# Kernel tuning notes

Measured on AMD Instinct MI355X. Metric: run time of the kernel, lower is better.

The kernel has to match this reference:

```python
import jax, jax.numpy as jnp
import numpy as np

EMBED = 8      # embed_dim == n_qubits == d_k (forced by reshapes in the source)
FFN = 2048
LN_EPS = 1e-5


def _layernorm(x, g, b):
    mu = jnp.mean(x, axis=-1, keepdims=True)
    var = jnp.mean(jnp.square(x - mu), axis=-1, keepdims=True)
    return (x - mu) * jax.lax.rsqrt(var + LN_EPS) * g + b


def _quantum_measure(theta):
    # RX(theta_i) on each wire of |0..0>, CNOT ladder 0->1->...->n-1,
    # then <Z_i>. Closed form: <Z_i> = prod_{j<=i} cos(theta_j).
    return jnp.cumprod(jnp.cos(theta), axis=-1)


def setup_inputs() -> dict:
    key = jax.random.key(0)
    ks = jax.random.split(key, 8)
    B, S = 32, 4096
    s_e = 1.0 / np.sqrt(EMBED)
    s_f = 1.0 / np.sqrt(FFN)
    return {
        "x": jax.random.normal(ks[0], (B, S, EMBED), jnp.float32),
        "Wq": jax.random.uniform(ks[1], (EMBED, EMBED), jnp.float32, -s_e, s_e),
        "Wo": jax.random.uniform(ks[2], (EMBED, EMBED), jnp.float32, -s_e, s_e),
        "W1": jax.random.uniform(ks[3], (FFN, EMBED), jnp.float32, -s_e, s_e),
        "b1": jax.random.uniform(ks[4], (FFN,), jnp.float32, -s_e, s_e),
        "W2": jax.random.uniform(ks[5], (EMBED, FFN), jnp.float32, -s_f, s_f),
        "b2": jax.random.uniform(ks[6], (EMBED,), jnp.float32, -s_f, s_f),
        "g1": jnp.ones((EMBED,), jnp.float32),
        "beta1": jnp.zeros((EMBED,), jnp.float32),
        "g2": jnp.ones((EMBED,), jnp.float32),
        "beta2": jnp.zeros((EMBED,), jnp.float32),
    }


def reference(x, Wq, Wo, W1, b1, W2, b2, g1, beta1, g2, beta2):
    # Quantum multi-head attention (num_heads=1, d_k=n_wires=8).
    # Note: k_proj / v_proj outputs are unused in the original forward.
    q = jnp.einsum("bse,fe->bsf", x, Wq)          # (B,S,E)
    attn = jnp.einsum("bse,fe->bsf", _quantum_measure(q), Wo)
    h = _layernorm(x + attn, g1, beta1)           # dropout is identity (eval)
    # Quantum feed-forward: measure -> linear1 -> relu -> linear2
    m = _quantum_measure(h)                       # (B,S,E)
    hid = jax.nn.relu(jnp.einsum("bse,fe->bsf", m, W1) + b1)  # (B,S,FFN)
    ffn = jnp.einsum("bsf,ef->bse", hid, W2) + b2
    return _layernorm(h + ffn, g2, beta2)
```

## Files before the change

### kernel.cpp

```cpp
#include <hip/hip_runtime.h>
#include <hip/hip_bf16.h>

#define FFN 2048
#define LN_EPS 1e-5f

typedef __attribute__((ext_vector_type(8))) short bf16x8;
typedef __attribute__((ext_vector_type(4))) float f32x4;

union FragU { bf16x8 v; unsigned u[4]; uint4 q; };

static __device__ __forceinline__ unsigned cvtpk(float lo, float hi) {
    unsigned r;
    asm("v_cvt_pk_bf16_f32 %0, %1, %2" : "=v"(r) : "v"(lo), "v"(hi));
    return r;
}

static __device__ __forceinline__ unsigned pkrelu(unsigned a, unsigned z) {
    unsigned r;
    asm("v_pk_max_f16 %0, %1, %2" : "=v"(r) : "v"(a), "v"(z));
    return r;
}

static __device__ __forceinline__ ushort to_bf16(float f) {
    unsigned u = __float_as_uint(f);
    u += 0x7fffu + ((u >> 16) & 1u);
    return (ushort)(u >> 16);
}

__global__ __launch_bounds__(256) void tbq_prep(
    const float* __restrict__ W1, const float* __restrict__ b1,
    const float* __restrict__ W2, uint4* __restrict__ ws)
{
    const int idx = blockIdx.x * 256 + threadIdx.x;
    ushort v[8] = {0,0,0,0,0,0,0,0};
    if (idx < 8192) {
        const int lane = idx & 63, s = (idx >> 6) & 1, cc = idx >> 7;
        const int c = lane & 15, g = lane >> 4;
        const int f = cc * 32 + s * 16 + c;
        if (g == 0) {
            #pragma unroll
            for (int j = 0; j < 8; ++j) v[j] = to_bf16(W1[f * 8 + j]);
        } else if (g == 1) {
            v[0] = to_bf16(b1[f]);
        }
    } else {
        const int i2 = idx - 8192;
        const int lane = i2 & 63, cc = i2 >> 6;
        const int c = lane & 15, g = lane >> 4;
        if (c < 8) {
            #pragma unroll
            for (int j = 0; j < 8; ++j) {
                const int fl = 4 * g + (j & 3) + 16 * (j >> 2);
                v[j] = to_bf16(W2[c * FFN + cc * 32 + fl]);
            }
        }
    }
    union { ushort s[8]; uint4 q; } pk;
    #pragma unroll
    for (int j = 0; j < 8; ++j) pk.s[j] = v[j];
    ws[idx] = pk.q;
}

__global__ __launch_bounds__(256) void tbq_mfma(
    const float* __restrict__ x,
    const float* __restrict__ Wq,
    const float* __restrict__ Wo,
    const float* __restrict__ b2,
    const float* __restrict__ g1,
    const float* __restrict__ beta1,
    const float* __restrict__ g2,
    const float* __restrict__ beta2,
    const uint4* __restrict__ ws,
    float* __restrict__ out)
{
    __shared__ __align__(16) uint4 mS[64];
    __shared__ __align__(16) float part[4][64][8];

    const int tid  = threadIdx.x;
    const int lane = tid & 63;
    const int wv   = tid >> 6;
    const int c    = lane & 15;
    const int g    = lane >> 4;
    const int t    = blockIdx.x * 64 + lane;

    const uint4* fw1 = ws + lane;
    const uint4* fw2 = ws + 8192 + lane;
    const int cc0 = wv * 16;

    FragU F0[2], F1[2], A2[2];
    F0[0].q = fw1[cc0 * 128];
    F1[0].q = fw1[cc0 * 128 + 64];
    A2[0].q = fw2[cc0 * 64];

    float h[8];
    if (wv == 0) {
        const float4* xr = (const float4*)(x + (size_t)t * 8);
        float4 xa = xr[0], xb = xr[1];
        float xv[8] = {xa.x, xa.y, xa.z, xa.w, xb.x, xb.y, xb.z, xb.w};

        float qm[8];
        {
            float cp = 1.0f;
            #pragma unroll
            for (int f = 0; f < 8; ++f) {
                float acc = 0.0f;
                #pragma unroll
                for (int e = 0; e < 8; ++e) acc += xv[e] * Wq[f * 8 + e];
                cp *= __cosf(acc);
                qm[f] = cp;
            }
        }
        float mu = 0.0f;
        #pragma unroll
        for (int f = 0; f < 8; ++f) {
            float acc = 0.0f;
            #pragma unroll
            for (int e = 0; e < 8; ++e) acc += qm[e] * Wo[f * 8 + e];
            h[f] = xv[f] + acc;
            mu += h[f];
        }
        mu *= 0.125f;
        float var = 0.0f;
        #pragma unroll
        for (int i = 0; i < 8; ++i) { float d = h[i] - mu; var += d * d; }
        var *= 0.125f;
        float rs = rsqrtf(var + LN_EPS);
        #pragma unroll
        for (int i = 0; i < 8; ++i) h[i] = (h[i] - mu) * rs * g1[i] + beta1[i];

        float m[8];
        {
            float cp = 1.0f;
            #pragma unroll
            for (int i = 0; i < 8; ++i) { cp *= __cosf(h[i]); m[i] = cp; }
        }
        uint4 mq;
        mq.x = cvtpk(m[0], m[1]); mq.y = cvtpk(m[2], m[3]);
        mq.z = cvtpk(m[4], m[5]); mq.w = cvtpk(m[6], m[7]);
        mS[lane] = mq;
    }
    __syncthreads();

    FragU B1[4];
    #pragma unroll
    for (int T = 0; T < 4; ++T) {
        uint4 mr = mS[T * 16 + c];
        B1[T].u[0] = (g == 0) ? mr.x : ((g == 1) ? 0x00003F80u : 0u);
        B1[T].u[1] = (g == 0) ? mr.y : 0u;
        B1[T].u[2] = (g == 0) ? mr.z : 0u;
        B1[T].u[3] = (g == 0) ? mr.w : 0u;
    }

    f32x4 acc[4] = {{0,0,0,0},{0,0,0,0},{0,0,0,0},{0,0,0,0}};
    const unsigned zz = 0u;

    #pragma unroll
    for (int i = 0; i < 16; ++i) {
        const int cur = i & 1, nxt = cur ^ 1;
        if (i < 15) {
            F0[nxt].q = fw1[(cc0 + i + 1) * 128];
            F1[nxt].q = fw1[(cc0 + i + 1) * 128 + 64];
            A2[nxt].q = fw2[(cc0 + i + 1) * 64];
        }
        #pragma unroll
        for (int T = 0; T < 4; ++T) {
            f32x4 z = {0, 0, 0, 0};
            f32x4 c0 = __builtin_amdgcn_mfma_f32_16x16x32_bf16(F0[cur].v, B1[T].v, z, 0, 0, 0);
            f32x4 c1 = __builtin_amdgcn_mfma_f32_16x16x32_bf16(F1[cur].v, B1[T].v, z, 0, 0, 0);
            FragU B2;
            B2.u[0] = pkrelu(cvtpk(c0[0], c0[1]), zz);
            B2.u[1] = pkrelu(cvtpk(c0[2], c0[3]), zz);
            B2.u[2] = pkrelu(cvtpk(c1[0], c1[1]), zz);
            B2.u[3] = pkrelu(cvtpk(c1[2], c1[3]), zz);
            acc[T] = __builtin_amdgcn_mfma_f32_16x16x32_bf16(A2[cur].v, B2.v, acc[T], 0, 0, 0);
        }
    }

    if (g < 2) {
        #pragma unroll
        for (int T = 0; T < 4; ++T) {
            *(f32x4*)&part[wv][T * 16 + c][4 * g] = acc[T];
        }
    }
    __syncthreads();

    if (wv == 0) {
        float ffnv[8];
        #pragma unroll
        for (int e = 0; e < 8; ++e)
            ffnv[e] = part[0][lane][e] + part[1][lane][e]
                    + part[2][lane][e] + part[3][lane][e];

        float o[8];
        float mu2 = 0.0f;
        #pragma unroll
        for (int i = 0; i < 8; ++i) { o[i] = h[i] + ffnv[i] + b2[i]; mu2 += o[i]; }
        mu2 *= 0.125f;
        float v2 = 0.0f;
        #pragma unroll
        for (int i = 0; i < 8; ++i) { float d = o[i] - mu2; v2 += d * d; }
        v2 *= 0.125f;
        float rs2 = rsqrtf(v2 + LN_EPS);

        float res[8];
        #pragma unroll
        for (int i = 0; i < 8; ++i) res[i] = (o[i] - mu2) * rs2 * g2[i] + beta2[i];

        float4* orow = (float4*)(out + (size_t)t * 8);
        orow[0] = make_float4(res[0], res[1], res[2], res[3]);
        orow[1] = make_float4(res[4], res[5], res[6], res[7]);
    }
}

extern "C" void kernel_launch(void* const* d_in, const int* in_sizes, int n_in,
                              void* d_out, int out_size, void* d_ws, size_t ws_size,
                              hipStream_t stream) {
    const float* x     = (const float*)d_in[0];
    const float* Wq    = (const float*)d_in[1];
    const float* Wo    = (const float*)d_in[2];
    const float* W1    = (const float*)d_in[3];
    const float* b1    = (const float*)d_in[4];
    const float* W2    = (const float*)d_in[5];
    const float* b2    = (const float*)d_in[6];
    const float* g1    = (const float*)d_in[7];
    const float* beta1 = (const float*)d_in[8];
    const float* g2    = (const float*)d_in[9];
    const float* beta2 = (const float*)d_in[10];
    float* out = (float*)d_out;
    uint4* ws = (uint4*)d_ws;

    tbq_prep<<<48, 256, 0, stream>>>(W1, b1, W2, ws);

    const int ntok = in_sizes[0] / 8;
    const int grid = ntok / 64;
    tbq_mfma<<<grid, 256, 0, stream>>>(x, Wq, Wo, b2, g1, beta1, g2, beta2, ws, out);
}
```

Measured before the change: 37.22 us.

## Split attention/LN1 prefix into a separate kernel to unblock MFMA waves

```diff
diff --git a/kernel.cpp b/kernel.cpp
--- a/kernel.cpp
+++ b/kernel.cpp
@@ -61,19 +61,75 @@
     ws[idx] = pk.q;
 }
 
-__global__ __launch_bounds__(256) void tbq_mfma(
+__global__ __launch_bounds__(64) void tbq_prefix(
     const float* __restrict__ x,
     const float* __restrict__ Wq,
     const float* __restrict__ Wo,
-    const float* __restrict__ b2,
     const float* __restrict__ g1,
     const float* __restrict__ beta1,
+    uint4* __restrict__ mws,
+    float* __restrict__ hout)
+{
+    const int t = blockIdx.x * 64 + threadIdx.x;
+    const float4* xr = (const float4*)(x + (size_t)t * 8);
+    float4 xa = xr[0], xb = xr[1];
+    float xv[8] = {xa.x, xa.y, xa.z, xa.w, xb.x, xb.y, xb.z, xb.w};
+
+    float qm[8];
+    {
+        float cp = 1.0f;
+        #pragma unroll
+        for (int f = 0; f < 8; ++f) {
+            float acc = 0.0f;
+            #pragma unroll
+            for (int e = 0; e < 8; ++e) acc += xv[e] * Wq[f * 8 + e];
+            cp *= __cosf(acc);
+            qm[f] = cp;
+        }
+    }
+    float h[8];
+    float mu = 0.0f;
+    #pragma unroll
+    for (int f = 0; f < 8; ++f) {
+        float acc = 0.0f;
+        #pragma unroll
+        for (int e = 0; e < 8; ++e) acc += qm[e] * Wo[f * 8 + e];
+        h[f] = xv[f] + acc;
+        mu += h[f];
+    }
+    mu *= 0.125f;
+    float var = 0.0f;
+    #pragma unroll
+    for (int i = 0; i < 8; ++i) { float d = h[i] - mu; var += d * d; }
+    var *= 0.125f;
+    float rs = rsqrtf(var + LN_EPS);
+    #pragma unroll
+    for (int i = 0; i < 8; ++i) h[i] = (h[i] - mu) * rs * g1[i] + beta1[i];
+
+    float m[8];
+    {
+        float cp = 1.0f;
+        #pragma unroll
+        for (int i = 0; i < 8; ++i) { cp *= __cosf(h[i]); m[i] = cp; }
+    }
+
+    uint4 mq;
+    mq.x = cvtpk(m[0], m[1]); mq.y = cvtpk(m[2], m[3]);
+    mq.z = cvtpk(m[4], m[5]); mq.w = cvtpk(m[6], m[7]);
+    mws[t] = mq;
+
+    float4* hr = (float4*)(hout + (size_t)t * 8);
+    hr[0] = make_float4(h[0], h[1], h[2], h[3]);
+    hr[1] = make_float4(h[4], h[5], h[6], h[7]);
+}
+
+__global__ __launch_bounds__(256) void tbq_mfma(
+    const float* __restrict__ b2,
     const float* __restrict__ g2,
     const float* __restrict__ beta2,
     const uint4* __restrict__ ws,
     float* __restrict__ out)
 {
-    __shared__ __align__(16) uint4 mS[64];
     __shared__ __align__(16) float part[4][64][8];
 
     const int tid  = threadIdx.x;
@@ -85,6 +141,7 @@
 
     const uint4* fw1 = ws + lane;
     const uint4* fw2 = ws + 8192 + lane;
+    const uint4* mws = ws + 12288;
     const int cc0 = wv * 16;
 
     FragU F0[2], F1[2], A2[2];
@@ -92,67 +149,22 @@
     F1[0].q = fw1[cc0 * 128 + 64];
     A2[0].q = fw2[cc0 * 64];
 
-    float h[8];
-    if (wv == 0) {
-        const float4* xr = (const float4*)(x + (size_t)t * 8);
-        float4 xa = xr[0], xb = xr[1];
-        float xv[8] = {xa.x, xa.y, xa.z, xa.w, xb.x, xb.y, xb.z, xb.w};
-
-        float qm[8];
-        {
-            float cp = 1.0f;
-            #pragma unroll
-            for (int f = 0; f < 8; ++f) {
-                float acc = 0.0f;
-                #pragma unroll
-                for (int e = 0; e < 8; ++e) acc += xv[e] * Wq[f * 8 + e];
-                cp *= __cosf(acc);
-                qm[f] = cp;
-            }
-        }
-        float mu = 0.0f;
-        #pragma unroll
-        for (int f = 0; f < 8; ++f) {
-            float acc = 0.0f;
-            #pragma unroll
-            for (int e = 0; e < 8; ++e) acc += qm[e] * Wo[f * 8 + e];
-            h[f] = xv[f] + acc;
-            mu += h[f];
-        }
-        mu *= 0.125f;
-        float var = 0.0f;
-        #pragma unroll
-        for (int i = 0; i < 8; ++i) { float d = h[i] - mu; var += d * d; }
-        var *= 0.125f;
-        float rs = rsqrtf(var + LN_EPS);
-        #pragma unroll
-        for (int i = 0; i < 8; ++i) h[i] = (h[i] - mu) * rs * g1[i] + beta1[i];
-
-        float m[8];
-        {
-            float cp = 1.0f;
-            #pragma unroll
-            for (int i = 0; i < 8; ++i) { cp *= __cosf(h[i]); m[i] = cp; }
-        }
-        uint4 mq;
-        mq.x = cvtpk(m[0], m[1]); mq.y = cvtpk(m[2], m[3]);
-        mq.z = cvtpk(m[4], m[5]); mq.w = cvtpk(m[6], m[7]);
-        mS[lane] = mq;
-    }
-    __syncthreads();
-
     FragU B1[4];
     #pragma unroll
     for (int T = 0; T < 4; ++T) {
-        uint4 mr = mS[T * 16 + c];
+        uint4 mr = mws[blockIdx.x * 64 + T * 16 + c];
         B1[T].u[0] = (g == 0) ? mr.x : ((g == 1) ? 0x00003F80u : 0u);
         B1[T].u[1] = (g == 0) ? mr.y : 0u;
         B1[T].u[2] = (g == 0) ? mr.z : 0u;
         B1[T].u[3] = (g == 0) ? mr.w : 0u;
     }
 
+    f32x4 z4 = {0.f, 0.f, 0.f, 0.f};
+    asm volatile("" : "+v"(z4));
+    unsigned zz = 0u;
+    asm volatile("" : "+v"(zz));
+
     f32x4 acc[4] = {{0,0,0,0},{0,0,0,0},{0,0,0,0},{0,0,0,0}};
-    const unsigned zz = 0u;
 
     #pragma unroll
     for (int i = 0; i < 16; ++i) {
@@ -164,9 +176,8 @@
         }
         #pragma unroll
         for (int T = 0; T < 4; ++T) {
-            f32x4 z = {0, 0, 0, 0};
-            f32x4 c0 = __builtin_amdgcn_mfma_f32_16x16x32_bf16(F0[cur].v, B1[T].v, z, 0, 0, 0);
-            f32x4 c1 = __builtin_amdgcn_mfma_f32_16x16x32_bf16(F1[cur].v, B1[T].v, z, 0, 0, 0);
+            f32x4 c0 = __builtin_amdgcn_mfma_f32_16x16x32_bf16(F0[cur].v, B1[T].v, z4, 0, 0, 0);
+            f32x4 c1 = __builtin_amdgcn_mfma_f32_16x16x32_bf16(F1[cur].v, B1[T].v, z4, 0, 0, 0);
             FragU B2;
             B2.u[0] = pkrelu(cvtpk(c0[0], c0[1]), zz);
             B2.u[1] = pkrelu(cvtpk(c0[2], c0[3]), zz);
@@ -190,6 +201,10 @@
         for (int e = 0; e < 8; ++e)
             ffnv[e] = part[0][lane][e] + part[1][lane][e]
                     + part[2][lane][e] + part[3][lane][e];
+
+        const float4* hr = (const float4*)(out + (size_t)t * 8);
+        float4 ha = hr[0], hb = hr[1];
+        float h[8] = {ha.x, ha.y, ha.z, ha.w, hb.x, hb.y, hb.z, hb.w};
 
         float o[8];
         float mu2 = 0.0f;
@@ -229,9 +244,9 @@
     float* out = (float*)d_out;
     uint4* ws = (uint4*)d_ws;
 
+    const int ntok = in_sizes[0] / 8;
+
     tbq_prep<<<48, 256, 0, stream>>>(W1, b1, W2, ws);
-
-    const int ntok = in_sizes[0] / 8;
-    const int grid = ntok / 64;
-    tbq_mfma<<<grid, 256, 0, stream>>>(x, Wq, Wo, b2, g1, beta1, g2, beta2, ws, out);
-}
+    tbq_prefix<<<ntok / 64, 64, 0, stream>>>(x, Wq, Wo, g1, beta1, ws + 12288, out);
+    tbq_mfma<<<ntok / 64, 256, 0, stream>>>(b2, g2, beta2, ws, out);
+}
```

Measured after the change: 38.63 us. +3.8%, slower.

## Double tokens per block and compact weight fragments with shared zero slot

Applied to the files above, without the earlier changes.

```diff
diff --git a/kernel.cpp b/kernel.cpp
--- a/kernel.cpp
+++ b/kernel.cpp
@@ -32,22 +32,26 @@
     const float* __restrict__ W2, uint4* __restrict__ ws)
 {
     const int idx = blockIdx.x * 256 + threadIdx.x;
+    if (idx >= 6336) return;
     ushort v[8] = {0,0,0,0,0,0,0,0};
-    if (idx < 8192) {
-        const int lane = idx & 63, s = (idx >> 6) & 1, cc = idx >> 7;
-        const int c = lane & 15, g = lane >> 4;
-        const int f = cc * 32 + s * 16 + c;
-        if (g == 0) {
-            #pragma unroll
-            for (int j = 0; j < 8; ++j) v[j] = to_bf16(W1[f * 8 + j]);
-        } else if (g == 1) {
-            v[0] = to_bf16(b1[f]);
+    if (idx < 4224) {
+        const int rec = idx / 33, r = idx % 33;
+        if (r) {
+            const int l32 = r - 1, c = l32 & 15, g = l32 >> 4;
+            const int s = rec & 1, cc = rec >> 1;
+            const int f = cc * 32 + s * 16 + c;
+            if (g == 0) {
+                #pragma unroll
+                for (int j = 0; j < 8; ++j) v[j] = to_bf16(W1[f * 8 + j]);
+            } else {
+                v[0] = to_bf16(b1[f]);
+            }
         }
     } else {
-        const int i2 = idx - 8192;
-        const int lane = i2 & 63, cc = i2 >> 6;
-        const int c = lane & 15, g = lane >> 4;
-        if (c < 8) {
+        const int i2 = idx - 4224;
+        const int rec = i2 / 33, r = i2 % 33;
+        if (r) {
+            const int l32 = r - 1, g = l32 >> 3, c = l32 & 7, cc = rec;
             #pragma unroll
             for (int j = 0; j < 8; ++j) {
                 const int fl = 4 * g + (j & 3) + 16 * (j >> 2);
@@ -73,27 +77,22 @@
     const uint4* __restrict__ ws,
     float* __restrict__ out)
 {
-    __shared__ __align__(16) uint4 mS[64];
-    __shared__ __align__(16) float part[4][64][8];
+    __shared__ __align__(16) uint4 mS[128];
+    __shared__ __align__(16) float part[4][128][8];
 
     const int tid  = threadIdx.x;
     const int lane = tid & 63;
     const int wv   = tid >> 6;
     const int c    = lane & 15;
     const int g    = lane >> 4;
-    const int t    = blockIdx.x * 64 + lane;
-
-    const uint4* fw1 = ws + lane;
-    const uint4* fw2 = ws + 8192 + lane;
-    const int cc0 = wv * 16;
-
-    FragU F0[2], F1[2], A2[2];
-    F0[0].q = fw1[cc0 * 128];
-    F1[0].q = fw1[cc0 * 128 + 64];
-    A2[0].q = fw2[cc0 * 64];
+    const int tok0 = blockIdx.x * 128;
+
+    const int o1 = (lane < 32) ? (1 + lane) : 0;
+    const int o2 = ((lane & 8) == 0) ? (1 + ((lane >> 4) << 3) + (lane & 7)) : 0;
 
     float h[8];
-    if (wv == 0) {
+    if (tid < 128) {
+        const int t = tok0 + tid;
         const float4* xr = (const float4*)(x + (size_t)t * 8);
         float4 xa = xr[0], xb = xr[1];
         float xv[8] = {xa.x, xa.y, xa.z, xa.w, xb.x, xb.y, xb.z, xb.w};
@@ -137,13 +136,13 @@
         uint4 mq;
         mq.x = cvtpk(m[0], m[1]); mq.y = cvtpk(m[2], m[3]);
         mq.z = cvtpk(m[4], m[5]); mq.w = cvtpk(m[6], m[7]);
-        mS[lane] = mq;
+        mS[tid] = mq;
     }
     __syncthreads();
 
-    FragU B1[4];
+    FragU B1[8];
     #pragma unroll
-    for (int T = 0; T < 4; ++T) {
+    for (int T = 0; T < 8; ++T) {
         uint4 mr = mS[T * 16 + c];
         B1[T].u[0] = (g == 0) ? mr.x : ((g == 1) ? 0x00003F80u : 0u);
         B1[T].u[1] = (g == 0) ? mr.y : 0u;
@@ -151,45 +150,53 @@
         B1[T].u[3] = (g == 0) ? mr.w : 0u;
     }
 
-    f32x4 acc[4] = {{0,0,0,0},{0,0,0,0},{0,0,0,0},{0,0,0,0}};
-    const unsigned zz = 0u;
-
-    #pragma unroll
+    f32x4 z4 = {0.f, 0.f, 0.f, 0.f};
+    asm volatile("" : "+v"(z4));
+    unsigned zz = 0u;
+    asm volatile("" : "+v"(zz));
+
+    f32x4 acc[8] = {{0,0,0,0},{0,0,0,0},{0,0,0,0},{0,0,0,0},
+                    {0,0,0,0},{0,0,0,0},{0,0,0,0},{0,0,0,0}};
+    const int cc0 = wv * 16;
+
+    #pragma unroll 4
     for (int i = 0; i < 16; ++i) {
-        const int cur = i & 1, nxt = cur ^ 1;
-        if (i < 15) {
-            F0[nxt].q = fw1[(cc0 + i + 1) * 128];
-            F1[nxt].q = fw1[(cc0 + i + 1) * 128 + 64];
-            A2[nxt].q = fw2[(cc0 + i + 1) * 64];
-        }
-        #pragma unroll
-        for (int T = 0; T < 4; ++T) {
-            f32x4 z = {0, 0, 0, 0};
-            f32x4 c0 = __builtin_amdgcn_mfma_f32_16x16x32_bf16(F0[cur].v, B1[T].v, z, 0, 0, 0);
-            f32x4 c1 = __builtin_amdgcn_mfma_f32_16x16x32_bf16(F1[cur].v, B1[T].v, z, 0, 0, 0);
+        const int cc = cc0 + i;
+        const uint4* r0 = ws + cc * 66;
+        const uint4* r1 = r0 + 33;
+        const uint4* r2 = ws + 4224 + cc * 33;
+        FragU F0, F1, A2;
+        F0.q = r0[o1];
+        F1.q = r1[o1];
+        A2.q = r2[o2];
+
+        #pragma unroll
+        for (int T = 0; T < 8; ++T) {
+            f32x4 c0 = __builtin_amdgcn_mfma_f32_16x16x32_bf16(F0.v, B1[T].v, z4, 0, 0, 0);
+            f32x4 c1 = __builtin_amdgcn_mfma_f32_16x16x32_bf16(F1.v, B1[T].v, z4, 0, 0, 0);
             FragU B2;
             B2.u[0] = pkrelu(cvtpk(c0[0], c0[1]), zz);
             B2.u[1] = pkrelu(cvtpk(c0[2], c0[3]), zz);
             B2.u[2] = pkrelu(cvtpk(c1[0], c1[1]), zz);
             B2.u[3] = pkrelu(cvtpk(c1[2], c1[3]), zz);
-            acc[T] = __builtin_amdgcn_mfma_f32_16x16x32_bf16(A2[cur].v, B2.v, acc[T], 0, 0, 0);
+            acc[T] = __builtin_amdgcn_mfma_f32_16x16x32_bf16(A2.v, B2.v, acc[T], 0, 0, 0);
         }
     }
 
     if (g < 2) {
         #pragma unroll
-        for (int T = 0; T < 4; ++T) {
+        for (int T = 0; T < 8; ++T) {
             *(f32x4*)&part[wv][T * 16 + c][4 * g] = acc[T];
         }
     }
     __syncthreads();
 
-    if (wv == 0) {
+    if (tid < 128) {
         float ffnv[8];
         #pragma unroll
         for (int e = 0; e < 8; ++e)
-            ffnv[e] = part[0][lane][e] + part[1][lane][e]
-                    + part[2][lane][e] + part[3][lane][e];
+            ffnv[e] = part[0][tid][e] + part[1][tid][e]
+                    + part[2][tid][e] + part[3][tid][e];
 
         float o[8];
         float mu2 = 0.0f;
@@ -206,7 +213,7 @@
         #pragma unroll
         for (int i = 0; i < 8; ++i) res[i] = (o[i] - mu2) * rs2 * g2[i] + beta2[i];
 
-        float4* orow = (float4*)(out + (size_t)t * 8);
+        float4* orow = (float4*)(out + (size_t)(tok0 + tid) * 8);
         orow[0] = make_float4(res[0], res[1], res[2], res[3]);
         orow[1] = make_float4(res[4], res[5], res[6], res[7]);
     }
@@ -229,9 +236,9 @@
     float* out = (float*)d_out;
     uint4* ws = (uint4*)d_ws;
 
-    tbq_prep<<<48, 256, 0, stream>>>(W1, b1, W2, ws);
+    tbq_prep<<<25, 256, 0, stream>>>(W1, b1, W2, ws);
 
     const int ntok = in_sizes[0] / 8;
-    const int grid = ntok / 64;
+    const int grid = ntok / 128;
     tbq_mfma<<<grid, 256, 0, stream>>>(x, Wq, Wo, b2, g1, beta1, g2, beta2, ws, out);
 }
```

Result: no change. 37.80 us (+1.5%).
